# Optimization experiments

Measured on AMD Instinct MI355X. Metric: run time of the kernel, lower is better.

The kernel has to match this reference:

```python
import jax, jax.numpy as jnp
import numpy as np

N_NODES = 50000
N_EDGES = 800000
N_GRAPHS = 1024
BN_EPS = 1e-5

def _linear_params(key, fan_in, fan_out):
    k1, k2 = jax.random.split(key)
    lim = 1.0 / np.sqrt(fan_in)
    w = jax.random.uniform(k1, (fan_in, fan_out), jnp.float32, -lim, lim)
    b = jax.random.uniform(k2, (fan_out,), jnp.float32, -lim, lim)
    return w, b


def setup_inputs() -> dict:
    key = jax.random.key(0)
    ks = jax.random.split(key, 16)
    x = jax.random.normal(ks[0], (N_NODES, 114), jnp.float32)
    edge_index = jax.random.randint(ks[1], (2, N_EDGES), 0, N_NODES, jnp.int64)
    batch = jnp.sort(jax.random.randint(ks[2], (N_NODES,), 0, N_GRAPHS, jnp.int64))
    w1a, b1a = _linear_params(ks[3], 114, 198)
    w1b, b1b = _linear_params(ks[4], 198, 198)
    w2a, b2a = _linear_params(ks[5], 198, 64)
    w2b, b2b = _linear_params(ks[6], 64, 64)
    w3a, b3a = _linear_params(ks[7], 64, 32)
    w3b, b3b = _linear_params(ks[8], 32, 32)
    fw1, fb1 = _linear_params(ks[9], 32, 16)
    fw2, fb2 = _linear_params(ks[10], 16, 8)
    ow, ob = _linear_params(ks[11], 8, 2)
    g1 = jnp.ones((198,), jnp.float32); be1 = jnp.zeros((198,), jnp.float32)
    g2 = jnp.ones((64,), jnp.float32); be2 = jnp.zeros((64,), jnp.float32)
    g3 = jnp.ones((32,), jnp.float32); be3 = jnp.zeros((32,), jnp.float32)
    return dict(x=x, edge_index=edge_index, batch=batch,
                w1a=w1a, b1a=b1a, w1b=w1b, b1b=b1b, g1=g1, be1=be1,
                w2a=w2a, b2a=b2a, w2b=w2b, b2b=b2b, g2=g2, be2=be2,
                w3a=w3a, b3a=b3a, w3b=w3b, b3b=b3b, g3=g3, be3=be3,
                fw1=fw1, fb1=fb1, fw2=fw2, fb2=fb2, ow=ow, ob=ob)


def _gin_conv(x, src, dst, wa, ba, wb, bb):
    # GINConv, eps=0: h_i = MLP((1+eps)*x_i + sum_{j->i} x_j)
    agg = jax.ops.segment_sum(x[src], dst, num_segments=N_NODES)
    h = x + agg
    h = jax.nn.relu(h @ wa + ba) @ wb + bb
    return h


def _batchnorm(h, gamma, beta):
    # training-mode BN over the node axis (biased variance, as torch)
    mean = jnp.mean(h, axis=0)
    var = jnp.var(h, axis=0)
    return (h - mean) * jax.lax.rsqrt(var + BN_EPS) * gamma + beta


def reference(x, edge_index, batch,
              w1a, b1a, w1b, b1b, g1, be1,
              w2a, b2a, w2b, b2b, g2, be2,
              w3a, b3a, w3b, b3b, g3, be3,
              fw1, fb1, fw2, fb2, ow, ob):
    src, dst = edge_index[0], edge_index[1]
    h = jax.nn.relu(_gin_conv(x, src, dst, w1a, b1a, w1b, b1b))
    h = _batchnorm(h, g1, be1)
    h = jax.nn.relu(_gin_conv(h, src, dst, w2a, b2a, w2b, b2b))
    h = _batchnorm(h, g2, be2)
    h = jax.nn.relu(_gin_conv(h, src, dst, w3a, b3a, w3b, b3b))
    h = _batchnorm(h, g3, be3)
    g = jax.ops.segment_sum(h, batch, num_segments=N_GRAPHS)  # global_add_pool
    g = jax.nn.relu(g @ fw1 + fb1)
    g = jax.nn.relu(g @ fw2 + fb2)
    return g @ ow + ob
```

## Files before the change

kernel.cpp:

```cpp
#include <hip/hip_runtime.h>

#define NODES  50000
#define EDGES  800000
#define GRAPHS 1024
#define P      200

#define SCAN_BLK 256
#define SCAN_NB  ((NODES + SCAN_BLK - 1) / SCAN_BLK)

typedef __attribute__((ext_vector_type(8))) short short8v;
typedef __attribute__((ext_vector_type(4))) short short4v;
typedef __attribute__((ext_vector_type(4))) float f32x4;

__device__ __forceinline__ ushort f2bf(float f) {
    uint u = __float_as_uint(f);
    u = u + 0x7FFFu + ((u >> 16) & 1u);
    return (ushort)(u >> 16);
}

__global__ void hist_kernel(const int* __restrict__ dst, int* __restrict__ deg,
                            const int* __restrict__ batch, int* __restrict__ cnt) {
    int e = blockIdx.x * blockDim.x + threadIdx.x;
    if (e < EDGES) atomicAdd(&deg[dst[e]], 1);
    if (e < NODES) atomicAdd(&cnt[batch[e]], 1);
}

__global__ void scan_part(const int* __restrict__ deg, int* __restrict__ part) {
    __shared__ int sh[SCAN_BLK];
    int t = threadIdx.x;
    int n = blockIdx.x * SCAN_BLK + t;
    sh[t] = (n < NODES) ? deg[n] : 0;
    __syncthreads();
    for (int off = SCAN_BLK / 2; off > 0; off >>= 1) {
        if (t < off) sh[t] += sh[t + off];
        __syncthreads();
    }
    if (t == 0) part[blockIdx.x] = sh[0];
}

__global__ void scan_scan(int* __restrict__ part) {
    __shared__ int sh[SCAN_BLK];
    int t = threadIdx.x;
    int v = (t < SCAN_NB) ? part[t] : 0;
    sh[t] = v;
    __syncthreads();
    for (int off = 1; off < SCAN_BLK; off <<= 1) {
        int u = 0;
        if (t >= off) u = sh[t - off];
        __syncthreads();
        if (t >= off) sh[t] += u;
        __syncthreads();
    }
    if (t < SCAN_NB) part[t] = sh[t] - v;
}

__global__ void scan_expand(const int* __restrict__ deg, const int* __restrict__ part,
                            int* __restrict__ rowstart, int* __restrict__ cursor) {
    __shared__ int sh[SCAN_BLK];
    int t = threadIdx.x;
    int n = blockIdx.x * SCAN_BLK + t;
    int v = (n < NODES) ? deg[n] : 0;
    sh[t] = v;
    __syncthreads();
    for (int off = 1; off < SCAN_BLK; off <<= 1) {
        int u = 0;
        if (t >= off) u = sh[t - off];
        __syncthreads();
        if (t >= off) sh[t] += u;
        __syncthreads();
    }
    int excl = sh[t] - v + part[blockIdx.x];
    if (n < NODES) {
        rowstart[n] = excl;
        cursor[n]   = excl;
        if (n == NODES - 1) rowstart[NODES] = excl + v;
    }
}

__global__ void scatter_kernel(const int* __restrict__ src, const int* __restrict__ dst,
                               int* __restrict__ cursor, int* __restrict__ csrc) {
    int e = blockIdx.x * blockDim.x + threadIdx.x;
    if (e < EDGES) {
        int p = atomicAdd(&cursor[dst[e]], 1);
        csrc[p] = src[e];
    }
}

__global__ void pad_all(const float* __restrict__ w1a, const float* __restrict__ w1b,
                        const float* __restrict__ w2a, const float* __restrict__ w2b,
                        const float* __restrict__ w3a, const float* __restrict__ w3b,
                        ushort* __restrict__ WF1, ushort* __restrict__ WF2,
                        ushort* __restrict__ WF3, ushort* __restrict__ WF4,
                        ushort* __restrict__ WF5, ushort* __restrict__ WF6) {
    int s = blockIdx.x * blockDim.x + threadIdx.x;
    const float* W; ushort* out; int K, N, NCH, CT, base;
    if      (s < 65536)  { W = w1a; out = WF1; K = 114; N = 198; NCH = 4; CT = 16; base = 0; }
    else if (s < 180224) { W = w1b; out = WF2; K = 198; N = 198; NCH = 7; CT = 16; base = 65536; }
    else if (s < 208896) { W = w2a; out = WF3; K = 198; N = 64;  NCH = 7; CT = 4;  base = 180224; }
    else if (s < 217088) { W = w2b; out = WF4; K = 64;  N = 64;  NCH = 2; CT = 4;  base = 208896; }
    else if (s < 225280) { W = w3a; out = WF5; K = 64;  N = 32;  NCH = 2; CT = 4;  base = 217088; }
    else if (s < 229376) { W = w3b; out = WF6; K = 32;  N = 32;  NCH = 1; CT = 4;  base = 225280; }
    else return;
    int idx = s - base;
    int half = NCH * CT * 512;
    int h = idx / half, r = idx % half;
    int j = r & 7, col = (r >> 3) & 15, kg = (r >> 7) & 3;
    int rest = r >> 9;
    int ct = rest % CT, c = rest / CT;
    int k = c * 32 + kg * 8 + j;
    int n = ct * 16 + col;
    float v = (k < K && n < N) ? W[k * N + n] : 0.0f;
    ushort hi = f2bf(v);
    if (h == 0) out[idx] = hi;
    else {
        float hf = __uint_as_float(((uint)hi) << 16);
        out[idx] = f2bf(v - hf);
    }
}

template<int D>
__global__ void csr_agg(const float* __restrict__ feat, int fpitch,
                        const int* __restrict__ rowstart, const int* __restrict__ csrc,
                        float* __restrict__ agg, int opitch) {
    int wid  = (blockIdx.x * blockDim.x + threadIdx.x) >> 6;
    int lane = threadIdx.x & 63;
    constexpr int UNR = 8;
    if constexpr (D == 32) {
        const int half = lane >> 5, sub = lane & 31;
        const int node = 2 * wid + half;
        const bool nact = node < NODES;
        const int r0 = nact ? rowstart[node] : 0;
        const int r1 = nact ? rowstart[node + 1] : 0;
        float s = 0.0f;
        for (int base = r0; base < r1; base += 32) {
            const int myidx = (base + sub < r1) ? csrc[base + sub] : 0;
            const int cnt = min(32, r1 - base);
            int t = 0;
            for (; t + UNR <= cnt; t += UNR) {
                const float* p[UNR];
#pragma unroll
                for (int u = 0; u < UNR; u++)
                    p[u] = feat + (size_t)__shfl(myidx, 32 * half + t + u) * fpitch;
                float v[UNR];
#pragma unroll
                for (int u = 0; u < UNR; u++) v[u] = p[u][sub];
                float acc = 0.0f;
#pragma unroll
                for (int u = 0; u < UNR; u++) acc += v[u];
                s += acc;
            }
            for (; t < cnt; t++) {
                const float* fp2 = feat + (size_t)__shfl(myidx, 32 * half + t) * fpitch;
                s += fp2[sub];
            }
        }
        if (nact) agg[(size_t)node * opitch + sub] = s;
    } else if constexpr (D == 114) {
        if (wid >= NODES) return;
        const int r0 = rowstart[wid], r1 = rowstart[wid + 1];
        const bool act = lane < 57;
        float sx = 0.0f, sy = 0.0f;
        for (int base = r0; base < r1; base += 64) {
            const int myidx = (base + lane < r1) ? csrc[base + lane] : 0;
            const int cnt = min(64, r1 - base);
            int t = 0;
            for (; t + UNR <= cnt; t += UNR) {
                const float2* p[UNR];
#pragma unroll
                for (int u = 0; u < UNR; u++)
                    p[u] = (const float2*)(feat + (size_t)__shfl(myidx, t + u) * fpitch);
                float2 v[UNR];
#pragma unroll
                for (int u = 0; u < UNR; u++) if (act) v[u] = p[u][lane];
                if (act) {
                    float ax = 0.0f, ay = 0.0f;
#pragma unroll
                    for (int u = 0; u < UNR; u++) { ax += v[u].x; ay += v[u].y; }
                    sx += ax; sy += ay;
                }
            }
            for (; t < cnt; t++) {
                const float2* fp2 = (const float2*)(feat + (size_t)__shfl(myidx, t) * fpitch);
                if (act) { float2 v = fp2[lane]; sx += v.x; sy += v.y; }
            }
        }
        if (act) *(float2*)(agg + (size_t)wid * opitch + 2 * lane) = make_float2(sx, sy);
    } else {
        if (wid >= NODES) return;
        const int r0 = rowstart[wid], r1 = rowstart[wid + 1];
        float s = 0.0f;
        for (int base = r0; base < r1; base += 64) {
            const int myidx = (base + lane < r1) ? csrc[base + lane] : 0;
            const int cnt = min(64, r1 - base);
            int t = 0;
            for (; t + UNR <= cnt; t += UNR) {
                const float* p[UNR];
#pragma unroll
                for (int u = 0; u < UNR; u++)
                    p[u] = feat + (size_t)__shfl(myidx, t + u) * fpitch;
                float v[UNR];
#pragma unroll
                for (int u = 0; u < UNR; u++)
                    if (lane < D) v[u] = p[u][lane];
                if (lane < D) {
                    float acc = 0.0f;
#pragma unroll
                    for (int u = 0; u < UNR; u++) acc += v[u];
                    s += acc;
                }
            }
            for (; t < cnt; t++) {
                const float* fp2 = feat + (size_t)__shfl(myidx, t) * fpitch;
                if (lane < D) s += fp2[lane];
            }
        }
        if (lane < D) agg[(size_t)wid * opitch + lane] = s;
    }
}

__launch_bounds__(256)
__global__ void gemm_fused_l1(const float* __restrict__ X,
                              const float* __restrict__ A2,
                              const ushort* __restrict__ WF1,
                              const float* __restrict__ B1,
                              const ushort* __restrict__ WF2,
                              const float* __restrict__ B2,
                              float* __restrict__ OUT,
                              float* __restrict__ gsum, float* __restrict__ gsq) {
    constexpr int K1   = 114;
    constexpr int NCH1 = 4;
    constexpr int NCH2 = 7;
    constexpr int CT   = 16;
    constexpr int CTW  = 4;
    constexpr int NN   = 198;

    __shared__ __align__(16) ushort A_lds[2][2][2][4][16][8];
    __shared__ __align__(16) ushort M_lds[2][NCH2][2][4][16][8];
    __shared__ float shSum[256];
    __shared__ float shSq [256];

    const int tid  = threadIdx.x;
    const int lane = tid & 63;
    const int wv   = tid >> 6;
    const int node0 = blockIdx.x * 32;

    for (int n = tid; n < 256; n += 256) { shSum[n] = 0.0f; shSq[n] = 0.0f; }

    const int sr  = tid >> 3;
    const int sc4 = (tid & 7) * 4;
    const int skg = sc4 >> 3;
    const int sj0 = sc4 & 7;
    const int gn  = node0 + sr;
    const size_t fstride1 = (size_t)NCH1 * CT * 512;
    const size_t fstride2 = (size_t)NCH2 * CT * 512;

    float xvA[4], a2vA[4], xvB[4], a2vB[4];

    auto loadA_A = [&](int c) {
        const int k0 = c * 32 + sc4;
#pragma unroll
        for (int j = 0; j < 4; j++) {
            int gk = k0 + j;
            bool ok = (gn < NODES && gk < K1);
            xvA[j]  = ok ? X[(size_t)gn * K1 + gk] : 0.0f;
            a2vA[j] = ok ? A2[(size_t)gn * P + gk] : 0.0f;
        }
    };
    auto loadA_B = [&](int c) {
        const int k0 = c * 32 + sc4;
#pragma unroll
        for (int j = 0; j < 4; j++) {
            int gk = k0 + j;
            bool ok = (gn < NODES && gk < K1);
            xvB[j]  = ok ? X[(size_t)gn * K1 + gk] : 0.0f;
            a2vB[j] = ok ? A2[(size_t)gn * P + gk] : 0.0f;
        }
    };
    auto cvtStore = [&](int buf, int c, const float* xv, const float* a2v) {
        const int k0 = c * 32 + sc4;
        short4v hv, lv;
#pragma unroll
        for (int j = 0; j < 4; j++) {
            int gk = k0 + j;
            float t = 0.0f;
            if (gn < NODES && gk < K1) t = xv[j] + a2v[j];
            ushort h = f2bf(t);
            float hf = __uint_as_float(((uint)h) << 16);
            ushort l = f2bf(t - hf);
            hv[j] = (short)h; lv[j] = (short)l;
        }
        *(short4v*)&A_lds[buf][0][sr >> 4][skg][sr & 15][sj0] = hv;
        *(short4v*)&A_lds[buf][1][sr >> 4][skg][sr & 15][sj0] = lv;
    };

    f32x4 acc1[2][CTW] = {};
    loadA_A(0);
    loadA_B(1);
    cvtStore(0, 0, xvA, a2vA);
    __syncthreads();

    const int kg = lane >> 4, rw = lane & 15;
#pragma unroll
    for (int c = 0; c < NCH1; c++) {
        const int buf = c & 1;
        if (c + 2 < NCH1) {
            if ((c & 1) == 0) loadA_A(c + 2);
            else              loadA_B(c + 2);
        }

        short8v ah[2], al[2];
#pragma unroll
        for (int rt = 0; rt < 2; rt++) {
            ah[rt] = *(const short8v*)&A_lds[buf][0][rt][kg][rw][0];
            al[rt] = *(const short8v*)&A_lds[buf][1][rt][kg][rw][0];
        }
        const size_t fb0 = ((size_t)(c * CT + wv * CTW)) * 512 + (size_t)lane * 8;
        short8v wh = *(const short8v*)(WF1 + fb0);
        short8v wl = *(const short8v*)(WF1 + fstride1 + fb0);
#pragma unroll
        for (int t = 0; t < CTW; t++) {
            short8v nwh, nwl;
            if (t + 1 < CTW) {
                const size_t fb = fb0 + (size_t)(t + 1) * 512;
                nwh = *(const short8v*)(WF1 + fb);
                nwl = *(const short8v*)(WF1 + fstride1 + fb);
            }
            __builtin_amdgcn_s_setprio(1);
#pragma unroll
            for (int rt = 0; rt < 2; rt++) {
                acc1[rt][t] = __builtin_amdgcn_mfma_f32_16x16x32_bf16(ah[rt], wh, acc1[rt][t], 0, 0, 0);
                acc1[rt][t] = __builtin_amdgcn_mfma_f32_16x16x32_bf16(al[rt], wh, acc1[rt][t], 0, 0, 0);
                acc1[rt][t] = __builtin_amdgcn_mfma_f32_16x16x32_bf16(ah[rt], wl, acc1[rt][t], 0, 0, 0);
            }
            __builtin_amdgcn_s_setprio(0);
            if (t + 1 < CTW) { wh = nwh; wl = nwl; }
        }
        if (c + 1 < NCH1) {
            if (((c + 1) & 1) == 0) cvtStore((c + 1) & 1, c + 1, xvA, a2vA);
            else                    cvtStore((c + 1) & 1, c + 1, xvB, a2vB);
        }
        __syncthreads();
    }

    const int mg = lane >> 4, colb = lane & 15;
#pragma unroll
    for (int t = 0; t < CTW; t++) {
        const int ct = wv * CTW + t;
        if (ct >= 14) continue;
        const int n = ct * 16 + colb;
        const float bn = (n < NN) ? B1[n] : 0.0f;
        const int c2 = n >> 5, kg2 = (n >> 3) & 3, j2 = n & 7;
#pragma unroll
        for (int rt = 0; rt < 2; rt++) {
#pragma unroll
            for (int j = 0; j < 4; j++) {
                float vv = fmaxf(acc1[rt][t][j] + bn, 0.0f);
                if (n >= NN) vv = 0.0f;
                ushort h = f2bf(vv);
                float hf = __uint_as_float(((uint)h) << 16);
                ushort l = f2bf(vv - hf);
                int row = mg * 4 + j;
                M_lds[0][c2][rt][kg2][row][j2] = h;
                M_lds[1][c2][rt][kg2][row][j2] = l;
            }
        }
    }
    __syncthreads();

    f32x4 acc2[2][CTW] = {};
#pragma unroll
    for (int c = 0; c < NCH2; c++) {
        short8v ah[2], al[2];
#pragma unroll
        for (int rt = 0; rt < 2; rt++) {
            ah[rt] = *(const short8v*)&M_lds[0][c][rt][kg][rw][0];
            al[rt] = *(const short8v*)&M_lds[1][c][rt][kg][rw][0];
        }
        const size_t fb0 = ((size_t)(c * CT + wv * CTW)) * 512 + (size_t)lane * 8;
        short8v wh = *(const short8v*)(WF2 + fb0);
        short8v wl = *(const short8v*)(WF2 + fstride2 + fb0);
#pragma unroll
        for (int t = 0; t < CTW; t++) {
            short8v nwh, nwl;
            if (t + 1 < CTW) {
                const size_t fb = fb0 + (size_t)(t + 1) * 512;
                nwh = *(const short8v*)(WF2 + fb);
                nwl = *(const short8v*)(WF2 + fstride2 + fb);
            }
            __builtin_amdgcn_s_setprio(1);
#pragma unroll
            for (int rt = 0; rt < 2; rt++) {
                acc2[rt][t] = __builtin_amdgcn_mfma_f32_16x16x32_bf16(ah[rt], wh, acc2[rt][t], 0, 0, 0);
                acc2[rt][t] = __builtin_amdgcn_mfma_f32_16x16x32_bf16(al[rt], wh, acc2[rt][t], 0, 0, 0);
                acc2[rt][t] = __builtin_amdgcn_mfma_f32_16x16x32_bf16(ah[rt], wl, acc2[rt][t], 0, 0, 0);
            }
            __builtin_amdgcn_s_setprio(0);
            if (t + 1 < CTW) { wh = nwh; wl = nwl; }
        }
    }

#pragma unroll
    for (int t = 0; t < CTW; t++) {
        const int ct = wv * CTW + t;
        const int n = ct * 16 + colb;
        const float bn = (n < NN) ? B2[n] : 0.0f;
        float psum = 0.0f, psq = 0.0f;
#pragma unroll
        for (int rt = 0; rt < 2; rt++) {
#pragma unroll
            for (int j = 0; j < 4; j++) {
                int m = node0 + rt * 16 + mg * 4 + j;
                float vv = fmaxf(acc2[rt][t][j] + bn, 0.0f);
                if (m < NODES && n < NN) {
                    OUT[(size_t)m * P + n] = vv;
                    psum += vv; psq += vv * vv;
                }
            }
        }
        if (n < NN) {
            atomicAdd(&shSum[n], psum);
            atomicAdd(&shSq[n], psq);
        }
    }
    __syncthreads();
    for (int n = tid; n < NN; n += 256) {
        atomicAdd(&gsum[n], shSum[n]);
        atomicAdd(&gsq[n], shSq[n]);
    }
}

template<int K, int N, bool ADD2, bool STATS, bool BNX, bool PRE, bool ACT,
         bool WRITE, bool POOL>
__launch_bounds__(256)
__global__ void gemm_mfma(const float* __restrict__ X, int xpitch,
                          const float* __restrict__ A2, int apitch,
                          const ushort* __restrict__ WF,
                          const float* __restrict__ B,
                          const float* __restrict__ PREB,
                          const float* __restrict__ bnsum, const float* __restrict__ bnsq,
                          const float* __restrict__ gamma, const float* __restrict__ beta,
                          float* __restrict__ OUT, int opitch,
                          float* __restrict__ gsum, float* __restrict__ gsq,
                          const int* __restrict__ batch, float* __restrict__ gpool) {
    constexpr int KP  = ((K + 31) / 32) * 32;
    constexpr int NCH = KP / 32;
    constexpr int NP  = ((N + 63) / 64) * 64;
    constexpr int CT  = NP / 16;
    constexpr int CTW = CT / 4;
    static_assert(CT % 4 == 0, "col tiles must split across 4 waves");

    __shared__ __align__(16) ushort A_lds[2][2][2][4][16][8];
    __shared__ float shSum[STATS ? NP : 4];
    __shared__ float shSq [STATS ? NP : 4];
    __shared__ float shSc [BNX ? 256 : 4];
    __shared__ float shSh [BNX ? 256 : 4];
    __shared__ float shPool[POOL ? 256 : 4];

    const int tid  = threadIdx.x;
    const int lane = tid & 63;
    const int wv   = tid >> 6;
    const int node0 = blockIdx.x * 32;

    int gfirst = 0, ng = 0;
    if (POOL) {
        gfirst = batch[min(node0, NODES - 1)];
        int glast = batch[min(node0 + 31, NODES - 1)];
        ng = glast - gfirst + 1;
        if (tid < 256) shPool[tid] = 0.0f;
    }
    if (STATS) {
        for (int n = tid; n < NP; n += 256) { shSum[n] = 0.0f; shSq[n] = 0.0f; }
    }
    if (BNX) {
        if (tid < K) {
            float mean = bnsum[tid] * (1.0f / NODES);
            float var  = bnsq[tid] * (1.0f / NODES) - mean * mean;
            var = var < 0.0f ? 0.0f : var;
            float sc = gamma[tid] * rsqrtf(var + 1e-5f);
            shSc[tid] = sc;
            shSh[tid] = beta[tid] - mean * sc;
        }
        __syncthreads();
    }

    f32x4 acc[2][CTW] = {};

    const int sr  = tid >> 3;
    const int sc4 = (tid & 7) * 4;
    const int skg = sc4 >> 3;
    const int sj0 = sc4 & 7;
    const int gn  = node0 + sr;
    const size_t fstride = (size_t)NCH * CT * 512;

    float xvA[4], xvB[4];
    float a2vA[ADD2 ? 4 : 1], a2vB[ADD2 ? 4 : 1];

    auto loadA_A = [&](int c) {
        const int k0 = c * 32 + sc4;
#pragma unroll
        for (int j = 0; j < 4; j++) {
            int gk = k0 + j;
            bool ok = (gn < NODES && gk < K);
            xvA[j] = ok ? X[(size_t)gn * xpitch + gk] : 0.0f;
            if (ADD2) a2vA[j] = ok ? A2[(size_t)gn * apitch + gk] : 0.0f;
        }
    };
    auto loadA_B = [&](int c) {
        const int k0 = c * 32 + sc4;
#pragma unroll
        for (int j = 0; j < 4; j++) {
            int gk = k0 + j;
            bool ok = (gn < NODES && gk < K);
            xvB[j] = ok ? X[(size_t)gn * xpitch + gk] : 0.0f;
            if (ADD2) a2vB[j] = ok ? A2[(size_t)gn * apitch + gk] : 0.0f;
        }
    };
    auto cvtCore = [&](int buf, int c, const float* xv, const float* a2v) {
        const int k0 = c * 32 + sc4;
        short4v hv, lv;
#pragma unroll
        for (int j = 0; j < 4; j++) {
            int gk = k0 + j;
            float t = 0.0f;
            if (gn < NODES && gk < K) {
                t = xv[j];
                if (BNX) t = fmaf(t, shSc[gk], shSh[gk]);
                if (ADD2) t += a2v[j];
                if (PRE)  t = fmaxf(t + PREB[gk], 0.0f);
            }
            ushort h = f2bf(t);
            float hf = __uint_as_float(((uint)h) << 16);
            ushort l = f2bf(t - hf);
            hv[j] = (short)h; lv[j] = (short)l;
        }
        *(short4v*)&A_lds[buf][0][sr >> 4][skg][sr & 15][sj0] = hv;
        *(short4v*)&A_lds[buf][1][sr >> 4][skg][sr & 15][sj0] = lv;
    };

    loadA_A(0);
    if (NCH > 1) loadA_B(1);
    cvtCore(0, 0, xvA, ADD2 ? a2vA : xvA);
    __syncthreads();

    const int kg = lane >> 4, rw = lane & 15;
#pragma unroll
    for (int c = 0; c < NCH; c++) {
        const int buf = c & 1;
        if (c + 2 < NCH) {
            if ((c & 1) == 0) loadA_A(c + 2);
            else              loadA_B(c + 2);
        }

        short8v ah[2], al[2];
#pragma unroll
        for (int rt = 0; rt < 2; rt++) {
            ah[rt] = *(const short8v*)&A_lds[buf][0][rt][kg][rw][0];
            al[rt] = *(const short8v*)&A_lds[buf][1][rt][kg][rw][0];
        }

        const size_t fb0 = ((size_t)(c * CT + wv * CTW)) * 512 + (size_t)lane * 8;
        short8v wh = *(const short8v*)(WF + fb0);
        short8v wl = *(const short8v*)(WF + fstride + fb0);
#pragma unroll
        for (int t = 0; t < CTW; t++) {
            short8v nwh, nwl;
            if (t + 1 < CTW) {
                const size_t fb = fb0 + (size_t)(t + 1) * 512;
                nwh = *(const short8v*)(WF + fb);
                nwl = *(const short8v*)(WF + fstride + fb);
            }
            __builtin_amdgcn_s_setprio(1);
#pragma unroll
            for (int rt = 0; rt < 2; rt++) {
                acc[rt][t] = __builtin_amdgcn_mfma_f32_16x16x32_bf16(ah[rt], wh, acc[rt][t], 0, 0, 0);
                acc[rt][t] = __builtin_amdgcn_mfma_f32_16x16x32_bf16(al[rt], wh, acc[rt][t], 0, 0, 0);
                acc[rt][t] = __builtin_amdgcn_mfma_f32_16x16x32_bf16(ah[rt], wl, acc[rt][t], 0, 0, 0);
            }
            __builtin_amdgcn_s_setprio(0);
            if (t + 1 < CTW) { wh = nwh; wl = nwl; }
        }

        if (c + 1 < NCH) {
            if (((c + 1) & 1) == 0) cvtCore((c + 1) & 1, c + 1, xvA, ADD2 ? a2vA : xvA);
            else                    cvtCore((c + 1) & 1, c + 1, xvB, ADD2 ? a2vB : xvB);
        }
        __syncthreads();
    }

    const int mg = lane >> 4, colb = lane & 15;
#pragma unroll
    for (int t = 0; t < CTW; t++) {
        const int ct = wv * CTW + t;
        const int n = ct * 16 + colb;
        const float bn = (ACT && n < N) ? B[n] : 0.0f;
        float psum = 0.0f, psq = 0.0f;
#pragma unroll
        for (int rt = 0; rt < 2; rt++) {
#pragma unroll
            for (int j = 0; j < 4; j++) {
                int m = node0 + rt * 16 + mg * 4 + j;
                float vv = ACT ? fmaxf(acc[rt][t][j] + bn, 0.0f) : acc[rt][t][j];
                if (m < NODES && n < N) {
                    if (WRITE) OUT[(size_t)m * opitch + n] = vv;
                    if (STATS) { psum += vv; psq += vv * vv; }
                    if (POOL) {
                        int g = batch[m];
                        if (ng <= 8) atomicAdd(&shPool[(g - gfirst) * 32 + n], vv);
                        else         atomicAdd(&gpool[g * 32 + n], vv);
                    }
                }
            }
        }
        if (STATS && n < N) {
            atomicAdd(&shSum[n], psum);
            atomicAdd(&shSq[n], psq);
        }
    }
    if (STATS || POOL) __syncthreads();
    if (STATS) {
        for (int n = tid; n < N; n += 256) {
            atomicAdd(&gsum[n], shSum[n]);
            atomicAdd(&gsq[n], shSq[n]);
        }
    }
    if (POOL && ng <= 8 && tid < ng * 32) {
        float v = shPool[tid];
        if (v != 0.0f) atomicAdd(&gpool[(gfirst + (tid >> 5)) * 32 + (tid & 31)], v);
    }
}

__global__ void head_kernel(const float* __restrict__ graw, const int* __restrict__ cnt,
                            const float* __restrict__ bnsum, const float* __restrict__ bnsq,
                            const float* __restrict__ gamma, const float* __restrict__ beta,
                            const float* __restrict__ fw1, const float* __restrict__ fb1,
                            const float* __restrict__ fw2, const float* __restrict__ fb2,
                            const float* __restrict__ ow, const float* __restrict__ ob,
                            float* __restrict__ out) {
    int gi = blockIdx.x * blockDim.x + threadIdx.x;
    if (gi >= GRAPHS) return;
    float cf = (float)cnt[gi];
    float v[32];
#pragma unroll
    for (int k = 0; k < 32; k++) {
        float mean = bnsum[k] * (1.0f / NODES);
        float var  = bnsq[k] * (1.0f / NODES) - mean * mean;
        var = var < 0.0f ? 0.0f : var;
        float sc = gamma[k] * rsqrtf(var + 1e-5f);
        float sh = beta[k] - mean * sc;
        v[k] = fmaf(graw[gi * 32 + k], sc, cf * sh);
    }
    float a1[16];
#pragma unroll
    for (int o = 0; o < 16; o++) {
        float s = fb1[o];
#pragma unroll
        for (int k = 0; k < 32; k++) s = fmaf(v[k], fw1[k * 16 + o], s);
        a1[o] = s > 0.0f ? s : 0.0f;
    }
    float a2[8];
#pragma unroll
    for (int o = 0; o < 8; o++) {
        float s = fb2[o];
#pragma unroll
        for (int k = 0; k < 16; k++) s = fmaf(a1[k], fw2[k * 8 + o], s);
        a2[o] = s > 0.0f ? s : 0.0f;
    }
#pragma unroll
    for (int o = 0; o < 2; o++) {
        float s = ob[o];
#pragma unroll
        for (int k = 0; k < 8; k++) s = fmaf(a2[k], ow[k * 2 + o], s);
        out[gi * 2 + o] = s;
    }
}

extern "C" void kernel_launch(void* const* d_in, const int* in_sizes, int n_in,
                              void* d_out, int out_size, void* d_ws, size_t ws_size,
                              hipStream_t stream) {
    const float* x     = (const float*)d_in[0];
    const int*   ei    = (const int*)d_in[1];
    const int*   batch = (const int*)d_in[2];
    const float *w1a = (const float*)d_in[3],  *b1a = (const float*)d_in[4];
    const float *w1b = (const float*)d_in[5],  *b1b = (const float*)d_in[6];
    const float *g1  = (const float*)d_in[7],  *be1 = (const float*)d_in[8];
    const float *w2a = (const float*)d_in[9],  *b2a = (const float*)d_in[10];
    const float *w2b = (const float*)d_in[11], *b2b = (const float*)d_in[12];
    const float *g2  = (const float*)d_in[13], *be2 = (const float*)d_in[14];
    const float *w3a = (const float*)d_in[15], *b3a = (const float*)d_in[16];
    const float *w3b = (const float*)d_in[17], *b3b = (const float*)d_in[18];
    const float *g3  = (const float*)d_in[19], *be3 = (const float*)d_in[20];
    const float *fw1 = (const float*)d_in[21], *fb1 = (const float*)d_in[22];
    const float *fw2 = (const float*)d_in[23], *fb2 = (const float*)d_in[24];
    const float *ow  = (const float*)d_in[25], *ob  = (const float*)d_in[26];
    const int* src = ei;
    const int* dst = ei + EDGES;

    float* ws  = (float*)d_ws;
    float* b0  = ws;
    float* b1  = ws + (size_t)NODES * P;
    float* Y2  = b1;
    float* AG2 = b1 + (size_t)NODES * 64;
    float* Y3  = b1;
    float* AG3 = b1 + (size_t)NODES * 32;

    int*   deg  = (int*)(ws + (size_t)2 * NODES * P);
    int*   cnt  = deg + NODES;
    float* SUM1 = (float*)(cnt + GRAPHS);
    float* SQ1  = SUM1 + 256;
    float* SUM2 = SQ1 + 256;
    float* SQ2  = SUM2 + 256;
    float* SUM3 = SQ2 + 256;
    float* SQ3  = SUM3 + 256;
    float* G    = SQ3 + 256;
    const size_t ZERO_ELEMS = (size_t)NODES + GRAPHS + 6 * 256 + (size_t)GRAPHS * 32;

    int* rowstart = (int*)(G + (size_t)GRAPHS * 32);
    int* cursor   = rowstart + NODES + 1;
    int* part     = cursor + NODES;
    int* csrc     = part + 256;
    uintptr_t wfp = ((uintptr_t)(csrc + EDGES) + 15) & ~(uintptr_t)15;
    ushort* WF1 = (ushort*)wfp;
    ushort* WF2 = WF1 + 65536;
    ushort* WF3 = WF2 + 114688;
    ushort* WF4 = WF3 + 28672;
    ushort* WF5 = WF4 + 8192;
    ushort* WF6 = WF5 + 8192;
    float* out = (float*)d_out;

    const int GBR  = (NODES + 31) / 32;
    const int AB   = (NODES * 64 + 255) / 256;
    const int AB2  = (((NODES + 1) / 2) * 64 + 255) / 256;
    const int EB   = (EDGES + 255) / 256;

    pad_all<<<(229376 + 255) / 256, 256, 0, stream>>>(w1a, w1b, w2a, w2b, w3a, w3b,
                                                      WF1, WF2, WF3, WF4, WF5, WF6);
    hipMemsetAsync(deg, 0, ZERO_ELEMS * sizeof(int), stream);

    hist_kernel<<<EB, 256, 0, stream>>>(dst, deg, batch, cnt);
    scan_part<<<SCAN_NB, SCAN_BLK, 0, stream>>>(deg, part);
    scan_scan<<<1, SCAN_BLK, 0, stream>>>(part);
    scan_expand<<<SCAN_NB, SCAN_BLK, 0, stream>>>(deg, part, rowstart, cursor);
    scatter_kernel<<<EB, 256, 0, stream>>>(src, dst, cursor, csrc);

    csr_agg<114><<<AB, 256, 0, stream>>>(x, 114, rowstart, csrc, b0, P);
    gemm_fused_l1<<<GBR, 256, 0, stream>>>(x, b0, WF1, b1a, WF2, b1b, b0, SUM1, SQ1);

    gemm_mfma<198, 64, false, false, true, false, false, true, false><<<GBR, 256, 0, stream>>>(
        b0, P, nullptr, 0, WF3, nullptr, nullptr, SUM1, SQ1, g1, be1,
        Y2, 64, nullptr, nullptr, nullptr, nullptr);
    csr_agg<64><<<AB, 256, 0, stream>>>(Y2, 64, rowstart, csrc, AG2, 64);
    gemm_mfma<64, 64, true, true, false, true, true, true, false><<<GBR, 256, 0, stream>>>(
        Y2, 64, AG2, 64, WF4, b2b, b2a, nullptr, nullptr, nullptr, nullptr,
        b0, 64, SUM2, SQ2, nullptr, nullptr);

    gemm_mfma<64, 32, false, false, true, false, false, true, false><<<GBR, 256, 0, stream>>>(
        b0, 64, nullptr, 0, WF5, nullptr, nullptr, SUM2, SQ2, g2, be2,
        Y3, 32, nullptr, nullptr, nullptr, nullptr);
    csr_agg<32><<<AB2, 256, 0, stream>>>(Y3, 32, rowstart, csrc, AG3, 32);
    gemm_mfma<32, 32, true, true, false, true, true, false, true><<<GBR, 256, 0, stream>>>(
        Y3, 32, AG3, 32, WF6, b3b, b3a, nullptr, nullptr, nullptr, nullptr,
        nullptr, 32, SUM3, SQ3, batch, G);

    head_kernel<<<(GRAPHS + 255) / 256, 256, 0, stream>>>(
        G, cnt, SUM3, SQ3, g3, be3, fw1, fb1, fw2, fb2, ow, ob, out);
}
```

Measured before the change: 404.7 us.

## Fold self term into layer-1 aggregation and prefetch weights across chunks

The 114-wide CSR aggregation now seeds each node's sum with its own features, so the fused layer-1 GEMM reads only the aggregated buffer instead of both x and the aggregate. The GEMM loops now prefetch the next chunk's weight fragments across chunk boundaries, and the second stage of the fused L1 kernel double-buffers its LDS operand loads in registers. This removes one global read stream from the first GEMM and hides weight and LDS load latency behind the MFMAs, at the cost of more live registers, which may lower occupancy.

```diff
diff --git a/kernel.cpp b/kernel.cpp
--- a/kernel.cpp
+++ b/kernel.cpp
@@ -160,6 +160,10 @@
         const int r0 = rowstart[wid], r1 = rowstart[wid + 1];
         const bool act = lane < 57;
         float sx = 0.0f, sy = 0.0f;
+        if (act) {
+            float2 own = ((const float2*)(feat + (size_t)wid * fpitch))[lane];
+            sx = own.x; sy = own.y;
+        }
         for (int base = r0; base < r1; base += 64) {
             const int myidx = (base + lane < r1) ? csrc[base + lane] : 0;
             const int cnt = min(64, r1 - base);
@@ -219,8 +223,7 @@
 }
 
 __launch_bounds__(256)
-__global__ void gemm_fused_l1(const float* __restrict__ X,
-                              const float* __restrict__ A2,
+__global__ void gemm_fused_l1(const float* __restrict__ A2,
                               const ushort* __restrict__ WF1,
                               const float* __restrict__ B1,
                               const ushort* __restrict__ WF2,
@@ -254,7 +257,7 @@
     const size_t fstride1 = (size_t)NCH1 * CT * 512;
     const size_t fstride2 = (size_t)NCH2 * CT * 512;
 
-    float xvA[4], a2vA[4], xvB[4], a2vB[4];
+    float xvA[4], xvB[4];
 
     auto loadA_A = [&](int c) {
         const int k0 = c * 32 + sc4;
@@ -262,8 +265,7 @@
         for (int j = 0; j < 4; j++) {
             int gk = k0 + j;
             bool ok = (gn < NODES && gk < K1);
-            xvA[j]  = ok ? X[(size_t)gn * K1 + gk] : 0.0f;
-            a2vA[j] = ok ? A2[(size_t)gn * P + gk] : 0.0f;
+            xvA[j] = ok ? A2[(size_t)gn * P + gk] : 0.0f;
         }
     };
     auto loadA_B = [&](int c) {
@@ -272,18 +274,16 @@
         for (int j = 0; j < 4; j++) {
             int gk = k0 + j;
             bool ok = (gn < NODES && gk < K1);
-            xvB[j]  = ok ? X[(size_t)gn * K1 + gk] : 0.0f;
-            a2vB[j] = ok ? A2[(size_t)gn * P + gk] : 0.0f;
+            xvB[j] = ok ? A2[(size_t)gn * P + gk] : 0.0f;
         }
     };
-    auto cvtStore = [&](int buf, int c, const float* xv, const float* a2v) {
+    auto cvtStore = [&](int buf, int c, const float* xv) {
         const int k0 = c * 32 + sc4;
         short4v hv, lv;
 #pragma unroll
         for (int j = 0; j < 4; j++) {
             int gk = k0 + j;
-            float t = 0.0f;
-            if (gn < NODES && gk < K1) t = xv[j] + a2v[j];
+            float t = (gn < NODES && gk < K1) ? xv[j] : 0.0f;
             ushort h = f2bf(t);
             float hf = __uint_as_float(((uint)h) << 16);
             ushort l = f2bf(t - hf);
@@ -296,50 +296,53 @@
     f32x4 acc1[2][CTW] = {};
     loadA_A(0);
     loadA_B(1);
-    cvtStore(0, 0, xvA, a2vA);
+    cvtStore(0, 0, xvA);
     __syncthreads();
 
     const int kg = lane >> 4, rw = lane & 15;
-#pragma unroll
-    for (int c = 0; c < NCH1; c++) {
-        const int buf = c & 1;
-        if (c + 2 < NCH1) {
-            if ((c & 1) == 0) loadA_A(c + 2);
-            else              loadA_B(c + 2);
-        }
-
-        short8v ah[2], al[2];
-#pragma unroll
-        for (int rt = 0; rt < 2; rt++) {
-            ah[rt] = *(const short8v*)&A_lds[buf][0][rt][kg][rw][0];
-            al[rt] = *(const short8v*)&A_lds[buf][1][rt][kg][rw][0];
-        }
-        const size_t fb0 = ((size_t)(c * CT + wv * CTW)) * 512 + (size_t)lane * 8;
-        short8v wh = *(const short8v*)(WF1 + fb0);
-        short8v wl = *(const short8v*)(WF1 + fstride1 + fb0);
-#pragma unroll
-        for (int t = 0; t < CTW; t++) {
-            short8v nwh, nwl;
-            if (t + 1 < CTW) {
-                const size_t fb = fb0 + (size_t)(t + 1) * 512;
-                nwh = *(const short8v*)(WF1 + fb);
-                nwl = *(const short8v*)(WF1 + fstride1 + fb);
-            }
-            __builtin_amdgcn_s_setprio(1);
+    {
+        size_t fbI = ((size_t)(wv * CTW)) * 512 + (size_t)lane * 8;
+        short8v wh = *(const short8v*)(WF1 + fbI);
+        short8v wl = *(const short8v*)(WF1 + fstride1 + fbI);
+#pragma unroll
+        for (int c = 0; c < NCH1; c++) {
+            const int buf = c & 1;
+            if (c + 2 < NCH1) {
+                if ((c & 1) == 0) loadA_A(c + 2);
+                else              loadA_B(c + 2);
+            }
+            short8v ah[2], al[2];
 #pragma unroll
             for (int rt = 0; rt < 2; rt++) {
-                acc1[rt][t] = __builtin_amdgcn_mfma_f32_16x16x32_bf16(ah[rt], wh, acc1[rt][t], 0, 0, 0);
-                acc1[rt][t] = __builtin_amdgcn_mfma_f32_16x16x32_bf16(al[rt], wh, acc1[rt][t], 0, 0, 0);
-                acc1[rt][t] = __builtin_amdgcn_mfma_f32_16x16x32_bf16(ah[rt], wl, acc1[rt][t], 0, 0, 0);
-            }
-            __builtin_amdgcn_s_setprio(0);
-            if (t + 1 < CTW) { wh = nwh; wl = nwl; }
-        }
-        if (c + 1 < NCH1) {
-            if (((c + 1) & 1) == 0) cvtStore((c + 1) & 1, c + 1, xvA, a2vA);
-            else                    cvtStore((c + 1) & 1, c + 1, xvB, a2vB);
-        }
-        __syncthreads();
+                ah[rt] = *(const short8v*)&A_lds[buf][0][rt][kg][rw][0];
+                al[rt] = *(const short8v*)&A_lds[buf][1][rt][kg][rw][0];
+            }
+#pragma unroll
+            for (int t = 0; t < CTW; t++) {
+                const int cn = (t + 1 < CTW) ? c : c + 1;
+                const int tn = (t + 1 < CTW) ? t + 1 : 0;
+                short8v nwh, nwl;
+                if (cn < NCH1) {
+                    const size_t fb = ((size_t)(cn * CT + wv * CTW + tn)) * 512 + (size_t)lane * 8;
+                    nwh = *(const short8v*)(WF1 + fb);
+                    nwl = *(const short8v*)(WF1 + fstride1 + fb);
+                }
+                __builtin_amdgcn_s_setprio(1);
+#pragma unroll
+                for (int rt = 0; rt < 2; rt++) {
+                    acc1[rt][t] = __builtin_amdgcn_mfma_f32_16x16x32_bf16(ah[rt], wh, acc1[rt][t], 0, 0, 0);
+                    acc1[rt][t] = __builtin_amdgcn_mfma_f32_16x16x32_bf16(al[rt], wh, acc1[rt][t], 0, 0, 0);
+                    acc1[rt][t] = __builtin_amdgcn_mfma_f32_16x16x32_bf16(ah[rt], wl, acc1[rt][t], 0, 0, 0);
+                }
+                __builtin_amdgcn_s_setprio(0);
+                if (cn < NCH1) { wh = nwh; wl = nwl; }
+            }
+            if (c + 1 < NCH1) {
+                if (((c + 1) & 1) == 0) cvtStore((c + 1) & 1, c + 1, xvA);
+                else                    cvtStore((c + 1) & 1, c + 1, xvB);
+            }
+            __syncthreads();
+        }
     }
 
     const int mg = lane >> 4, colb = lane & 15;
@@ -368,34 +371,48 @@
     __syncthreads();
 
     f32x4 acc2[2][CTW] = {};
-#pragma unroll
-    for (int c = 0; c < NCH2; c++) {
-        short8v ah[2], al[2];
-#pragma unroll
-        for (int rt = 0; rt < 2; rt++) {
-            ah[rt] = *(const short8v*)&M_lds[0][c][rt][kg][rw][0];
-            al[rt] = *(const short8v*)&M_lds[1][c][rt][kg][rw][0];
-        }
-        const size_t fb0 = ((size_t)(c * CT + wv * CTW)) * 512 + (size_t)lane * 8;
-        short8v wh = *(const short8v*)(WF2 + fb0);
-        short8v wl = *(const short8v*)(WF2 + fstride2 + fb0);
-#pragma unroll
-        for (int t = 0; t < CTW; t++) {
-            short8v nwh, nwl;
-            if (t + 1 < CTW) {
-                const size_t fb = fb0 + (size_t)(t + 1) * 512;
-                nwh = *(const short8v*)(WF2 + fb);
-                nwl = *(const short8v*)(WF2 + fstride2 + fb);
-            }
-            __builtin_amdgcn_s_setprio(1);
+    {
+        auto loadM = [&](int c, short8v (&ah)[2], short8v (&al)[2]) {
 #pragma unroll
             for (int rt = 0; rt < 2; rt++) {
-                acc2[rt][t] = __builtin_amdgcn_mfma_f32_16x16x32_bf16(ah[rt], wh, acc2[rt][t], 0, 0, 0);
-                acc2[rt][t] = __builtin_amdgcn_mfma_f32_16x16x32_bf16(al[rt], wh, acc2[rt][t], 0, 0, 0);
-                acc2[rt][t] = __builtin_amdgcn_mfma_f32_16x16x32_bf16(ah[rt], wl, acc2[rt][t], 0, 0, 0);
-            }
-            __builtin_amdgcn_s_setprio(0);
-            if (t + 1 < CTW) { wh = nwh; wl = nwl; }
+                ah[rt] = *(const short8v*)&M_lds[0][c][rt][kg][rw][0];
+                al[rt] = *(const short8v*)&M_lds[1][c][rt][kg][rw][0];
+            }
+        };
+        short8v ahE[2], alE[2], ahO[2], alO[2];
+        loadM(0, ahE, alE);
+        size_t fbI = ((size_t)(wv * CTW)) * 512 + (size_t)lane * 8;
+        short8v wh = *(const short8v*)(WF2 + fbI);
+        short8v wl = *(const short8v*)(WF2 + fstride2 + fbI);
+#pragma unroll
+        for (int c = 0; c < NCH2; c++) {
+            const bool even = (c & 1) == 0;
+            if (c + 1 < NCH2) {
+                if (even) loadM(c + 1, ahO, alO);
+                else      loadM(c + 1, ahE, alE);
+            }
+#pragma unroll
+            for (int t = 0; t < CTW; t++) {
+                const int cn = (t + 1 < CTW) ? c : c + 1;
+                const int tn = (t + 1 < CTW) ? t + 1 : 0;
+                short8v nwh, nwl;
+                if (cn < NCH2) {
+                    const size_t fb = ((size_t)(cn * CT + wv * CTW + tn)) * 512 + (size_t)lane * 8;
+                    nwh = *(const short8v*)(WF2 + fb);
+                    nwl = *(const short8v*)(WF2 + fstride2 + fb);
+                }
+                __builtin_amdgcn_s_setprio(1);
+#pragma unroll
+                for (int rt = 0; rt < 2; rt++) {
+                    const short8v a_h = even ? ahE[rt] : ahO[rt];
+                    const short8v a_l = even ? alE[rt] : alO[rt];
+                    acc2[rt][t] = __builtin_amdgcn_mfma_f32_16x16x32_bf16(a_h, wh, acc2[rt][t], 0, 0, 0);
+                    acc2[rt][t] = __builtin_amdgcn_mfma_f32_16x16x32_bf16(a_l, wh, acc2[rt][t], 0, 0, 0);
+                    acc2[rt][t] = __builtin_amdgcn_mfma_f32_16x16x32_bf16(a_h, wl, acc2[rt][t], 0, 0, 0);
+                }
+                __builtin_amdgcn_s_setprio(0);
+                if (cn < NCH2) { wh = nwh; wl = nwl; }
+            }
         }
     }
 
@@ -540,6 +557,9 @@
     loadA_A(0);
     if (NCH > 1) loadA_B(1);
     cvtCore(0, 0, xvA, ADD2 ? a2vA : xvA);
+    size_t fbI = ((size_t)(wv * CTW)) * 512 + (size_t)lane * 8;
+    short8v wh = *(const short8v*)(WF + fbI);
+    short8v wl = *(const short8v*)(WF + fstride + fbI);
     __syncthreads();
 
     const int kg = lane >> 4, rw = lane & 15;
@@ -558,14 +578,13 @@
             al[rt] = *(const short8v*)&A_lds[buf][1][rt][kg][rw][0];
         }
 
-        const size_t fb0 = ((size_t)(c * CT + wv * CTW)) * 512 + (size_t)lane * 8;
-        short8v wh = *(const short8v*)(WF + fb0);
-        short8v wl = *(const short8v*)(WF + fstride + fb0);
 #pragma unroll
         for (int t = 0; t < CTW; t++) {
+            const int cn = (t + 1 < CTW) ? c : c + 1;
+            const int tn = (t + 1 < CTW) ? t + 1 : 0;
             short8v nwh, nwl;
-            if (t + 1 < CTW) {
-                const size_t fb = fb0 + (size_t)(t + 1) * 512;
+            if (cn < NCH) {
+                const size_t fb = ((size_t)(cn * CT + wv * CTW + tn)) * 512 + (size_t)lane * 8;
                 nwh = *(const short8v*)(WF + fb);
                 nwl = *(const short8v*)(WF + fstride + fb);
             }
@@ -577,7 +596,7 @@
                 acc[rt][t] = __builtin_amdgcn_mfma_f32_16x16x32_bf16(ah[rt], wl, acc[rt][t], 0, 0, 0);
             }
             __builtin_amdgcn_s_setprio(0);
-            if (t + 1 < CTW) { wh = nwh; wl = nwl; }
+            if (cn < NCH) { wh = nwh; wl = nwl; }
         }
 
         if (c + 1 < NCH) {
@@ -743,7 +762,7 @@
     scatter_kernel<<<EB, 256, 0, stream>>>(src, dst, cursor, csrc);
 
     csr_agg<114><<<AB, 256, 0, stream>>>(x, 114, rowstart, csrc, b0, P);
-    gemm_fused_l1<<<GBR, 256, 0, stream>>>(x, b0, WF1, b1a, WF2, b1b, b0, SUM1, SQ1);
+    gemm_fused_l1<<<GBR, 256, 0, stream>>>(b0, WF1, b1a, WF2, b1b, b0, SUM1, SQ1);
 
     gemm_mfma<198, 64, false, false, true, false, false, true, false><<<GBR, 256, 0, stream>>>(
         b0, P, nullptr, 0, WF3, nullptr, nullptr, SUM1, SQ1, g1, be1,
```

Result: no change. 406.9 us (+0.6%).
